# Kernel tuning notes

Hardware: AMD Instinct MI355X
Metric: run time of the kernel (lower is better)

## Reference

```python
import jax, jax.numpy as jnp
import numpy as np

C = 64
CQ = C // 8


def setup_inputs() -> dict:
    key = jax.random.key(0)
    ks = jax.random.split(key, 8)
    scale = 0.05
    x = jax.random.normal(ks[0], (4, C, 64, 64), dtype=jnp.float32)
    Wq = jax.random.normal(ks[1], (CQ, C), dtype=jnp.float32) * scale
    bq = jax.random.normal(ks[2], (CQ,), dtype=jnp.float32) * scale
    Wk = jax.random.normal(ks[3], (CQ, C), dtype=jnp.float32) * scale
    bk = jax.random.normal(ks[4], (CQ,), dtype=jnp.float32) * scale
    Wv = jax.random.normal(ks[5], (C, C), dtype=jnp.float32) * scale
    bv = jax.random.normal(ks[6], (C,), dtype=jnp.float32) * scale
    gamma = jnp.zeros((1,), dtype=jnp.float32) + 0.5  # nonzero so output depends on attention
    return {"x": x, "Wq": Wq, "bq": bq, "Wk": Wk, "bk": bk, "Wv": Wv, "bv": bv, "gamma": gamma}


def reference(x, Wq, bq, Wk, bk, Wv, bv, gamma):
    bs, c, h, w = x.shape
    hw = h * w
    xf = x.reshape(bs, c, hw)  # [b, c, hw]
    # 1x1 convs == per-pixel linear over channels
    Q = jnp.einsum('oc,bcn->bon', Wq, xf) + bq[None, :, None]  # [b, c/8, hw]
    K = jnp.einsum('oc,bcn->bon', Wk, xf) + bk[None, :, None]  # [b, c/8, hw]
    V = jnp.einsum('oc,bcn->bon', Wv, xf) + bv[None, :, None]  # [b, c, hw]
    # attention = softmax(Q^T K, axis=-1), NO scaling (matches source)
    scores = jnp.einsum('bqn,bqm->bnm', Q, K)  # [b, hw, hw]
    attn = jax.nn.softmax(scores, axis=-1)
    out = jnp.einsum('bcm,bmn->bcn', V, attn)  # torch.bmm(V_, attention)
    out = out.reshape(bs, c, h, w)
    return gamma[0] * out + x
```

## Files before the change

### kernel.cpp

```cpp
#include <hip/hip_runtime.h>


constexpr int Bn = 4, Cc = 64, Q8 = 8, Np = 4096;
constexpr int QK_STR = 32;
constexpr int PSTR = 40;
constexpr int NSL = 8;

typedef float f32x4 __attribute__((ext_vector_type(4)));
typedef short short8 __attribute__((ext_vector_type(8)));

__device__ inline unsigned int f2bf(float x) {
    unsigned int u = __float_as_uint(x);
    u += 0x7fff + ((u >> 16) & 1);
    return u >> 16;
}
__device__ inline float bf2f(unsigned int u) { return __uint_as_float(u << 16); }

__device__ inline unsigned cvt_pk_bf16(float a, float b) {
    unsigned r;
    asm("v_cvt_pk_bf16_f32 %0, %1, %2" : "=v"(r) : "v"(a), "v"(b));
    return r;
}
__device__ inline float exp2g(float x) {
#if __has_builtin(__builtin_amdgcn_exp2f)
    return __builtin_amdgcn_exp2f(x);
#else
    return exp2f(x);
#endif
}
__device__ inline float log2g(float x) {
#if __has_builtin(__builtin_amdgcn_logf)
    return __builtin_amdgcn_logf(x);
#else
    return log2f(x);
#endif
}

__global__ __launch_bounds__(64) void qkv_v3(
    const float* __restrict__ x,
    const float* __restrict__ Wq, const float* __restrict__ bq,
    const float* __restrict__ Wk, const float* __restrict__ bk,
    const float* __restrict__ Wv, const float* __restrict__ bv,
    unsigned short* __restrict__ Qp, unsigned short* __restrict__ Kp,
    unsigned short* __restrict__ Vb)
{
    const int lane = threadIdx.x;
    const int gpos = blockIdx.x * 64;
    const int os = blockIdx.y;
    const int b = gpos >> 12, n = (gpos & (Np - 1)) + lane;
    const float LOG2E = 1.4426950408889634f;

    float xv[Cc];
    const float* xp = x + (size_t)(b * Cc) * Np + n;
    #pragma unroll
    for (int c = 0; c < Cc; c++) xv[c] = xp[(size_t)c * Np];

    if (os <= 1) {
        const float* W = (os == 0) ? Wq : Wk;
        const float* bb = (os == 0) ? bq : bk;
        const float sc = (os == 0) ? LOG2E : 1.0f;
        unsigned pk[4];
        #pragma unroll
        for (int p = 0; p < 4; p++) {
            float a0 = bb[2 * p], a1 = bb[2 * p + 1];
            #pragma unroll
            for (int c = 0; c < Cc; c++) {
                a0 += W[(2 * p) * Cc + c] * xv[c];
                a1 += W[(2 * p + 1) * Cc + c] * xv[c];
            }
            pk[p] = f2bf(a0 * sc) | (f2bf(a1 * sc) << 16);
        }
        unsigned short* row = (os == 0 ? Qp : Kp) + (size_t)(b * Np + n) * QK_STR;
        *(uint4*)row = make_uint4(pk[0], pk[1], pk[2], pk[3]);
        *(uint4*)(row + 8)  = make_uint4(0, 0, 0, 0);
        *(uint4*)(row + 16) = make_uint4(0, 0, 0, 0);
        *(uint4*)(row + 24) = make_uint4(0, 0, 0, 0);
        const int vbase = 60 + (os == 0 ? 2 : 0);
        #pragma unroll
        for (int o = 0; o < 2; o++) {
            const int vr = vbase + o;
            float a = bv[vr];
            #pragma unroll
            for (int c = 0; c < Cc; c++) a += Wv[vr * Cc + c] * xv[c];
            Vb[(size_t)(b * Cc + vr) * Np + n] = (unsigned short)f2bf(a);
        }
    } else {
        const int vbase = (os - 2) * 10;
        #pragma unroll
        for (int o = 0; o < 10; o++) {
            const int vr = vbase + o;
            float a = bv[vr];
            #pragma unroll
            for (int c = 0; c < Cc; c++) a += Wv[vr * Cc + c] * xv[c];
            Vb[(size_t)(b * Cc + vr) * Np + n] = (unsigned short)f2bf(a);
        }
    }
}

__global__ __launch_bounds__(256) void zsum_v3(
    const unsigned short* __restrict__ Qp, const unsigned short* __restrict__ Kp,
    float* __restrict__ ZP)
{
    const int tid = threadIdx.x, w = tid >> 6, lane = tid & 63;
    const int quad = lane >> 4, l15 = lane & 15;
    const int bz = blockIdx.z, ns = blockIdx.y;
    const int m0 = blockIdx.x * 64 + w * 16;

    short8 qa = *(const short8*)&Qp[((size_t)(bz * Np + m0 + l15)) * QK_STR + quad * 8];
    const unsigned short* kbase = Kp + (size_t)bz * Np * QK_STR;
    const int nbase = ns * (Np / NSL);

    float z0 = 0.f, z1 = 0.f, z2 = 0.f, z3 = 0.f;
    #pragma unroll 4
    for (int nt = 0; nt < Np / NSL; nt += 16) {
        short8 kb = *(const short8*)
            &kbase[(size_t)(nbase + nt + l15) * QK_STR + quad * 8];
        f32x4 s = __builtin_amdgcn_mfma_f32_16x16x32_bf16(
            qa, kb, f32x4{0.f, 0.f, 0.f, 0.f}, 0, 0, 0);
        z0 += exp2g(s[0]); z1 += exp2g(s[1]);
        z2 += exp2g(s[2]); z3 += exp2g(s[3]);
    }
    #pragma unroll
    for (int mask = 1; mask < 16; mask <<= 1) {
        z0 += __shfl_xor(z0, mask); z1 += __shfl_xor(z1, mask);
        z2 += __shfl_xor(z2, mask); z3 += __shfl_xor(z3, mask);
    }
    if (l15 == 0) {
        float4 v = make_float4(z0, z1, z2, z3);
        *(float4*)&ZP[((size_t)(bz * NSL + ns)) * Np + m0 + quad * 4] = v;
    }
}

__global__ __launch_bounds__(256) void zred(
    const float* __restrict__ ZP, float* __restrict__ Lg)
{
    int i = blockIdx.x * 256 + threadIdx.x;
    int b = i >> 12, m = i & (Np - 1);
    float z = 0.f;
    #pragma unroll
    for (int s = 0; s < NSL; s++) z += ZP[((size_t)(b * NSL + s)) * Np + m];
    Lg[(size_t)b * Np + m] = -log2g(z);
}

__global__ __launch_bounds__(256) void attn_v4(
    const unsigned short* __restrict__ Qp, const unsigned short* __restrict__ Kp,
    const unsigned short* __restrict__ Vb, const float* __restrict__ Lg,
    unsigned short* __restrict__ PO, int Ms, int SL)
{
    __shared__ unsigned short Plds[128 * PSTR];
    const int tid = threadIdx.x, w = tid >> 6, lane = tid & 63;
    const int quad = lane >> 4, l15 = lane & 15;
    const int bz = blockIdx.z, by = blockIdx.y, nb = blockIdx.x * 128;

    short8 kf[2];
    #pragma unroll
    for (int t = 0; t < 2; t++) {
        int n = nb + (2 * w + t) * 16 + l15;
        kf[t] = *(const short8*)&Kp[((size_t)(bz * Np + n)) * QK_STR + quad * 8];
    }
    f32x4 acc[4][2];
    #pragma unroll
    for (int ct = 0; ct < 4; ct++)
        #pragma unroll
        for (int t = 0; t < 2; t++) acc[ct][t] = f32x4{0.f, 0.f, 0.f, 0.f};

    const int m_base = by * Ms;
    for (int mi = 0; mi < Ms; mi += 32) {
        const int m0 = m_base + mi;
        #pragma unroll
        for (int mt = 0; mt < 2; mt++) {
            short8 qa = *(const short8*)
                &Qp[((size_t)(bz * Np + m0 + mt * 16 + l15)) * QK_STR + quad * 8];
            f32x4 Lc = *(const f32x4*)
                &Lg[(size_t)bz * Np + m0 + mt * 16 + quad * 4];
            #pragma unroll
            for (int t = 0; t < 2; t++) {
                f32x4 s = __builtin_amdgcn_mfma_f32_16x16x32_bf16(qa, kf[t], Lc, 0, 0, 0);
                unsigned p01 = cvt_pk_bf16(exp2g(s[0]), exp2g(s[1]));
                unsigned p23 = cvt_pk_bf16(exp2g(s[2]), exp2g(s[3]));
                int nl = (2 * w + t) * 16 + l15;
                *(uint2*)&Plds[nl * PSTR + mt * 16 + quad * 4] = make_uint2(p01, p23);
            }
        }
        short8 pb[2];
        #pragma unroll
        for (int t = 0; t < 2; t++)
            pb[t] = *(const short8*)&Plds[(w * 32 + t * 16 + l15) * PSTR + quad * 8];
        #pragma unroll
        for (int ct = 0; ct < 4; ct++) {
            short8 ua = *(const short8*)
                &Vb[((size_t)(bz * Cc + ct * 16 + l15)) * Np + m0 + quad * 8];
            #pragma unroll
            for (int t = 0; t < 2; t++)
                acc[ct][t] = __builtin_amdgcn_mfma_f32_16x16x32_bf16(
                    ua, pb[t], acc[ct][t], 0, 0, 0);
        }
    }
    unsigned short* po = PO + ((size_t)((bz * SL + by) * Cc)) * Np + nb;
    #pragma unroll
    for (int ct = 0; ct < 4; ct++)
        #pragma unroll
        for (int t = 0; t < 2; t++) {
            int c = ct * 16 + quad * 4, n = w * 32 + t * 16 + l15;
            #pragma unroll
            for (int r = 0; r < 4; r++)
                po[(size_t)(c + r) * Np + n] = (unsigned short)f2bf(acc[ct][t][r]);
        }
}

__global__ __launch_bounds__(256) void combine_kernel(
    const unsigned short* __restrict__ PO, const float* __restrict__ x,
    const float* __restrict__ gamma, float* __restrict__ out, int sl2)
{
    int idx8 = (blockIdx.x * 256 + threadIdx.x) * 8;
    int b = idx8 >> 18;
    int c = (idx8 >> 12) & 63;
    int n = idx8 & (Np - 1);
    float o[8];
    #pragma unroll
    for (int i = 0; i < 8; i++) o[i] = 0.f;
    for (int sl = 0; sl < sl2; ++sl) {
        uint4 u = *(const uint4*)&PO[(size_t)((b * sl2 + sl) * Cc + c) * Np + n];
        o[0] += bf2f(u.x & 0xffff); o[1] += bf2f(u.x >> 16);
        o[2] += bf2f(u.y & 0xffff); o[3] += bf2f(u.y >> 16);
        o[4] += bf2f(u.z & 0xffff); o[5] += bf2f(u.z >> 16);
        o[6] += bf2f(u.w & 0xffff); o[7] += bf2f(u.w >> 16);
    }
    float g = gamma[0];
    float4 x0 = *(const float4*)&x[idx8];
    float4 x1 = *(const float4*)&x[idx8 + 4];
    float4 r0 = make_float4(g * o[0] + x0.x, g * o[1] + x0.y,
                            g * o[2] + x0.z, g * o[3] + x0.w);
    float4 r1 = make_float4(g * o[4] + x1.x, g * o[5] + x1.y,
                            g * o[6] + x1.z, g * o[7] + x1.w);
    *(float4*)&out[idx8] = r0;
    *(float4*)&out[idx8 + 4] = r1;
}

extern "C" void kernel_launch(void* const* d_in, const int* in_sizes, int n_in,
                              void* d_out, int out_size, void* d_ws, size_t ws_size,
                              hipStream_t stream)
{
    const float* x     = (const float*)d_in[0];
    const float* Wq    = (const float*)d_in[1];
    const float* bq    = (const float*)d_in[2];
    const float* Wk    = (const float*)d_in[3];
    const float* bk    = (const float*)d_in[4];
    const float* Wv    = (const float*)d_in[5];
    const float* bv    = (const float*)d_in[6];
    const float* gamma = (const float*)d_in[7];
    float* out = (float*)d_out;

    unsigned short* Qp = (unsigned short*)d_ws;
    unsigned short* Kp = Qp + (size_t)Bn * Np * QK_STR;
    unsigned short* Vb = Kp + (size_t)Bn * Np * QK_STR;
    float* Lg   = (float*)(Vb + (size_t)Bn * Cc * Np);
    float* ZP   = Lg + (size_t)Bn * Np;
    unsigned short* PO = (unsigned short*)(ZP + (size_t)Bn * NSL * Np);

    size_t baseB = (size_t)Bn * Np * QK_STR * 2 * 2 + (size_t)Bn * Cc * Np * 2
                 + (size_t)Bn * Np * 4 + (size_t)Bn * NSL * Np * 4;
    int SL = 8;
    while (SL > 1 && baseB + (size_t)Bn * SL * Cc * Np * 2 > ws_size) SL >>= 1;

    qkv_v3<<<dim3(Bn * Np / 64, 8), 64, 0, stream>>>(x, Wq, bq, Wk, bk, Wv, bv,
                                                     Qp, Kp, Vb);
    zsum_v3<<<dim3(Np / 64, NSL, Bn), 256, 0, stream>>>(Qp, Kp, ZP);
    zred<<<Bn * Np / 256, 256, 0, stream>>>(ZP, Lg);
    attn_v4<<<dim3(Np / 128, SL, Bn), 256, 0, stream>>>(Qp, Kp, Vb, Lg,
                                                        PO, Np / SL, SL);
    combine_kernel<<<Bn * Cc * Np / (256 * 8), 256, 0, stream>>>(PO, x, gamma, out, SL);
}
```

Before: 147.2 us.

## Compute QKV projection with bf16 MFMA over an LDS-transposed x tile

Replaces the scalar per-pixel FMA projection kernel with an MFMA version. Each block stages a 64x64 tile of x into LDS as bf16 in transposed form, and each output tile of 16 rows (Q+K together, or 16 V rows) is computed with two 16x16x32 bf16 MFMAs per 16 pixels. The grid shrinks from 8 to 5 output slices. It also quantizes x and the weights to bf16 before accumulation, which lowers precision compared with the fp32 FMAs, and the V stores become scattered 2-byte writes.

```diff
diff --git a/kernel.cpp b/kernel.cpp
--- a/kernel.cpp
+++ b/kernel.cpp
@@ -5,6 +5,7 @@
 constexpr int QK_STR = 32;
 constexpr int PSTR = 40;
 constexpr int NSL = 8;
+constexpr int XSTR = 72;
 
 typedef float f32x4 __attribute__((ext_vector_type(4)));
 typedef short short8 __attribute__((ext_vector_type(8)));
@@ -36,7 +37,7 @@
 #endif
 }
 
-__global__ __launch_bounds__(64) void qkv_v3(
+__global__ __launch_bounds__(64) void qkv_mfma(
     const float* __restrict__ x,
     const float* __restrict__ Wq, const float* __restrict__ bq,
     const float* __restrict__ Wk, const float* __restrict__ bk,
@@ -44,55 +45,78 @@
     unsigned short* __restrict__ Qp, unsigned short* __restrict__ Kp,
     unsigned short* __restrict__ Vb)
 {
+    __shared__ unsigned short xT[64 * XSTR];
     const int lane = threadIdx.x;
+    const int quad = lane >> 4, l15 = lane & 15;
     const int gpos = blockIdx.x * 64;
-    const int os = blockIdx.y;
-    const int b = gpos >> 12, n = (gpos & (Np - 1)) + lane;
+    const int ot = blockIdx.y;
+    const int b = gpos >> 12, n0 = gpos & (Np - 1);
     const float LOG2E = 1.4426950408889634f;
 
-    float xv[Cc];
-    const float* xp = x + (size_t)(b * Cc) * Np + n;
-    #pragma unroll
-    for (int c = 0; c < Cc; c++) xv[c] = xp[(size_t)c * Np];
-
-    if (os <= 1) {
-        const float* W = (os == 0) ? Wq : Wk;
-        const float* bb = (os == 0) ? bq : bk;
-        const float sc = (os == 0) ? LOG2E : 1.0f;
-        unsigned pk[4];
-        #pragma unroll
-        for (int p = 0; p < 4; p++) {
-            float a0 = bb[2 * p], a1 = bb[2 * p + 1];
-            #pragma unroll
-            for (int c = 0; c < Cc; c++) {
-                a0 += W[(2 * p) * Cc + c] * xv[c];
-                a1 += W[(2 * p + 1) * Cc + c] * xv[c];
+    {
+        const float* xrow = x + (size_t)(b * Cc + lane) * Np + n0;
+        #pragma unroll
+        for (int i4 = 0; i4 < 16; i4++) {
+            float4 v = *(const float4*)&xrow[i4 * 4];
+            int nb4 = i4 * 4;
+            xT[(nb4 + 0) * XSTR + lane] = (unsigned short)f2bf(v.x);
+            xT[(nb4 + 1) * XSTR + lane] = (unsigned short)f2bf(v.y);
+            xT[(nb4 + 2) * XSTR + lane] = (unsigned short)f2bf(v.z);
+            xT[(nb4 + 3) * XSTR + lane] = (unsigned short)f2bf(v.w);
+        }
+    }
+    __syncthreads();
+
+    const float* Wrow;
+    if (ot == 0) Wrow = (l15 < 8) ? (Wq + l15 * Cc) : (Wk + (l15 - 8) * Cc);
+    else         Wrow = Wv + ((ot - 1) * 16 + l15) * Cc;
+    short8 wa[2];
+    #pragma unroll
+    for (int kf = 0; kf < 2; kf++) {
+        #pragma unroll
+        for (int jj = 0; jj < 8; jj++)
+            wa[kf][jj] = (short)f2bf(Wrow[kf * 32 + quad * 8 + jj]);
+    }
+    float bias[4];
+    if (ot == 0) {
+        const float* bb = (quad < 2) ? bq : bk;
+        int off = (quad & 1) * 4;
+        #pragma unroll
+        for (int r = 0; r < 4; r++) bias[r] = bb[off + r];
+    } else {
+        #pragma unroll
+        for (int r = 0; r < 4; r++) bias[r] = bv[(ot - 1) * 16 + quad * 4 + r];
+    }
+
+    #pragma unroll
+    for (int nt = 0; nt < 4; nt++) {
+        short8 xb0 = *(const short8*)&xT[(nt * 16 + l15) * XSTR + quad * 8];
+        short8 xb1 = *(const short8*)&xT[(nt * 16 + l15) * XSTR + 32 + quad * 8];
+        f32x4 cc = __builtin_amdgcn_mfma_f32_16x16x32_bf16(
+            wa[0], xb0, f32x4{0.f, 0.f, 0.f, 0.f}, 0, 0, 0);
+        cc = __builtin_amdgcn_mfma_f32_16x16x32_bf16(wa[1], xb1, cc, 0, 0, 0);
+        int n = n0 + nt * 16 + l15;
+        if (ot == 0) {
+            float v0 = cc[0] + bias[0], v1 = cc[1] + bias[1];
+            float v2 = cc[2] + bias[2], v3 = cc[3] + bias[3];
+            if (quad < 2) { v0 *= LOG2E; v1 *= LOG2E; v2 *= LOG2E; v3 *= LOG2E; }
+            unsigned p01 = cvt_pk_bf16(v0, v1), p23 = cvt_pk_bf16(v2, v3);
+            unsigned short* rowp = (quad < 2 ? Qp : Kp)
+                + ((size_t)(b * Np + n)) * QK_STR;
+            *(uint2*)(rowp + (quad & 1) * 4) = make_uint2(p01, p23);
+            if ((quad & 1) == 0) {
+                *(uint4*)(rowp + 8) = make_uint4(0, 0, 0, 0);
+            } else {
+                *(uint4*)(rowp + 16) = make_uint4(0, 0, 0, 0);
+                *(uint4*)(rowp + 24) = make_uint4(0, 0, 0, 0);
             }
-            pk[p] = f2bf(a0 * sc) | (f2bf(a1 * sc) << 16);
-        }
-        unsigned short* row = (os == 0 ? Qp : Kp) + (size_t)(b * Np + n) * QK_STR;
-        *(uint4*)row = make_uint4(pk[0], pk[1], pk[2], pk[3]);
-        *(uint4*)(row + 8)  = make_uint4(0, 0, 0, 0);
-        *(uint4*)(row + 16) = make_uint4(0, 0, 0, 0);
-        *(uint4*)(row + 24) = make_uint4(0, 0, 0, 0);
-        const int vbase = 60 + (os == 0 ? 2 : 0);
-        #pragma unroll
-        for (int o = 0; o < 2; o++) {
-            const int vr = vbase + o;
-            float a = bv[vr];
-            #pragma unroll
-            for (int c = 0; c < Cc; c++) a += Wv[vr * Cc + c] * xv[c];
-            Vb[(size_t)(b * Cc + vr) * Np + n] = (unsigned short)f2bf(a);
-        }
-    } else {
-        const int vbase = (os - 2) * 10;
-        #pragma unroll
-        for (int o = 0; o < 10; o++) {
-            const int vr = vbase + o;
-            float a = bv[vr];
-            #pragma unroll
-            for (int c = 0; c < Cc; c++) a += Wv[vr * Cc + c] * xv[c];
-            Vb[(size_t)(b * Cc + vr) * Np + n] = (unsigned short)f2bf(a);
+        } else {
+            #pragma unroll
+            for (int r = 0; r < 4; r++) {
+                int vr = (ot - 1) * 16 + quad * 4 + r;
+                Vb[(size_t)(b * Cc + vr) * Np + n] =
+                    (unsigned short)f2bf(cc[r] + bias[r]);
+            }
         }
     }
 }
@@ -263,8 +287,8 @@
     int SL = 8;
     while (SL > 1 && baseB + (size_t)Bn * SL * Cc * Np * 2 > ws_size) SL >>= 1;
 
-    qkv_v3<<<dim3(Bn * Np / 64, 8), 64, 0, stream>>>(x, Wq, bq, Wk, bk, Wv, bv,
-                                                     Qp, Kp, Vb);
+    qkv_mfma<<<dim3(Bn * Np / 64, 5), 64, 0, stream>>>(x, Wq, bq, Wk, bk, Wv, bv,
+                                                       Qp, Kp, Vb);
     zsum_v3<<<dim3(Np / 64, NSL, Bn), 256, 0, stream>>>(Qp, Kp, ZP);
     zred<<<Bn * Np / 256, 256, 0, stream>>>(ZP, Lg);
     attn_v4<<<dim3(Np / 128, SL, Bn), 256, 0, stream>>>(Qp, Kp, Vb, Lg,
```

Result: faster. 141.4 us (-4.0%).
